# Performance work log

Measured on AMD Instinct MI355X. Metric: run time of the kernel, lower is better.

The kernel has to match this reference:

```python
import jax, jax.numpy as jnp
import numpy as np

B, N, C = 4, 2048, 1024
H = 16
D = C // H  # head dim = 64

def setup_inputs() -> dict:
    key = jax.random.key(0)
    k1, k2, k3 = jax.random.split(key, 3)
    x = jax.random.normal(k1, (B, N, C), dtype=jnp.float32)
    w_attn = jax.random.normal(k2, (C, 3 * C), dtype=jnp.float32) * (C ** -0.5)
    w_proj = jax.random.normal(k3, (C, C), dtype=jnp.float32) * (C ** -0.5)
    return {"x": x, "w_attn": w_attn, "w_proj": w_proj}

def reference(x, w_attn, w_proj):
    # fused QKV projection (bias=False)
    qkv = jnp.einsum('bnc,cf->bnf', x, w_attn)            # [B,N,3C]
    q, k, v = jnp.split(qkv, 3, axis=-1)                  # each [B,N,C]
    # [B,H,N,D]
    q = q.reshape(B, N, H, D).transpose(0, 2, 1, 3)
    k = k.reshape(B, N, H, D).transpose(0, 2, 1, 3)
    v = v.reshape(B, N, H, D).transpose(0, 2, 1, 3)
    # scaled dot-product attention, non-causal, no mask, dropout_p=0
    scale = 1.0 / jnp.sqrt(jnp.asarray(D, dtype=q.dtype))
    scores = jnp.einsum('bhqd,bhkd->bhqk', q, k) * scale  # [B,H,N,N]
    attn = jax.nn.softmax(scores, axis=-1)
    y = jnp.einsum('bhqk,bhkd->bhqd', attn, v)            # [B,H,N,D]
    y = y.transpose(0, 2, 1, 3).reshape(B, N, C)
    # output projection (bias=False); resid dropout is identity at p=0
    return jnp.einsum('bnc,co->bno', y, w_proj)
```

## Files before the change

kernel.cpp:

```cpp
#include <hip/hip_runtime.h>
#include <hip/hip_bf16.h>

typedef __hip_bfloat16 bf16;
typedef short short8 __attribute__((ext_vector_type(8)));
typedef float f32x4 __attribute__((ext_vector_type(4)));
typedef float f32x16 __attribute__((ext_vector_type(16)));

#define GLOBAL_AS __attribute__((address_space(1)))
#define LDS_AS __attribute__((address_space(3)))

__device__ inline unsigned short f2bf(float x) {
    union { float f; unsigned u; } v; v.f = x;
    unsigned r = v.u + 0x7fffu + ((v.u >> 16) & 1u);
    return (unsigned short)(r >> 16);
}

__device__ inline unsigned pkbf(float a, float b) {
    float2 f; f.x = a; f.y = b;
    union { __hip_bfloat162 h; unsigned u; } c;
    c.h = __float22bfloat162_rn(f);
    return c.u;
}

__device__ inline float fast_exp2(float x) {
#if __has_builtin(__builtin_amdgcn_exp2f)
    return __builtin_amdgcn_exp2f(x);
#else
    return exp2f(x);
#endif
}

__device__ inline void async16(const void* g, void* l) {
    __builtin_amdgcn_global_load_lds((const GLOBAL_AS void*)g, (LDS_AS void*)l, 16, 0, 0);
}


__global__ __launch_bounds__(256) void cvt_f32_bf16(const float* __restrict__ in,
                                                    unsigned short* __restrict__ out, int n4) {
    int i = blockIdx.x * 256 + threadIdx.x;
    if (i < n4) {
        float4 v = ((const float4*)in)[i];
        ushort4 o;
        o.x = f2bf(v.x); o.y = f2bf(v.y); o.z = f2bf(v.z); o.w = f2bf(v.w);
        ((ushort4*)out)[i] = o;
    }
}

__global__ __launch_bounds__(256) void transpose_bf16(const float* __restrict__ in,
                                                      unsigned short* __restrict__ out,
                                                      int R, int Cc) {
    __shared__ float s[32][33];
    int tx = threadIdx.x & 31, ty = threadIdx.x >> 5;
    int c0 = blockIdx.x * 32, r0 = blockIdx.y * 32;
#pragma unroll
    for (int i = 0; i < 4; i++)
        s[ty + i * 8][tx] = in[(size_t)(r0 + ty + i * 8) * Cc + c0 + tx];
    __syncthreads();
#pragma unroll
    for (int i = 0; i < 4; i++)
        out[(size_t)(c0 + ty + i * 8) * R + r0 + tx] = f2bf(s[tx][ty + i * 8]);
}


template <int MODE>
__global__ __launch_bounds__(256) void gemm_bf16(const bf16* __restrict__ A,
                                                 const bf16* __restrict__ Bt,
                                                 unsigned short* __restrict__ outQ,
                                                 unsigned short* __restrict__ outK,
                                                 unsigned short* __restrict__ outV,
                                                 float* __restrict__ outF, float qscale) {
    const int KD = 1024;
    __shared__ __align__(16) char smem[34816];
    bf16* sA = (bf16*)smem;
    bf16* sB = (bf16*)(smem + 16384);
    const int t = threadIdx.x;
    const int w = t >> 6, lane = t & 63, l15 = lane & 15, qd = lane >> 4;
    const int bn = blockIdx.x, bm = blockIdx.y;
    const int wm = (w >> 1) * 64, wn = (w & 1) * 64;
    const int sw = l15 & 7;

    f32x4 acc[4][4];
#pragma unroll
    for (int i = 0; i < 4; i++)
#pragma unroll
        for (int j = 0; j < 4; j++) acc[i][j] = (f32x4){0.f, 0.f, 0.f, 0.f};

    const int rsub = lane >> 3;
    const int csrc = ((lane & 7) ^ rsub) << 3;
    const bf16* Ab = A + (size_t)(bm * 128 + w * 32 + rsub) * KD + csrc;
    const bf16* Bb = Bt + (size_t)(bn * 128 + w * 32 + rsub) * KD + csrc;
    bf16* sAw = sA + (w * 32) * 64;
    bf16* sBw = sB + (w * 32) * 64;

    for (int kt = 0; kt < 16; ++kt) {
#pragma unroll
        for (int j = 0; j < 4; ++j) {
            async16(Ab + (size_t)(j * 8) * KD + kt * 64, sAw + j * 512);
            async16(Bb + (size_t)(j * 8) * KD + kt * 64, sBw + j * 512);
        }
        __syncthreads();
#pragma unroll
        for (int ks = 0; ks < 2; ++ks) {
            const int cphys = (((ks * 4 + qd) ^ sw) << 3);
            short8 af[4], bfv[4];
#pragma unroll
            for (int mi = 0; mi < 4; mi++)
                af[mi] = *(const short8*)&sA[(wm + mi * 16 + l15) * 64 + cphys];
#pragma unroll
            for (int ni = 0; ni < 4; ni++)
                bfv[ni] = *(const short8*)&sB[(wn + ni * 16 + l15) * 64 + cphys];
#pragma unroll
            for (int mi = 0; mi < 4; mi++)
#pragma unroll
                for (int ni = 0; ni < 4; ni++)
                    acc[mi][ni] = __builtin_amdgcn_mfma_f32_16x16x32_bf16(af[mi], bfv[ni],
                                                                          acc[mi][ni], 0, 0, 0);
        }
        __syncthreads();
    }

    if (MODE == 0) {
        unsigned short* sC = (unsigned short*)smem;
        const int part = bn >> 3;
        const int hb = (bn & 7) * 2;
        if (part < 2) {
            const float sc = (part == 0) ? qscale : 1.0f;
            unsigned short* dst = (part == 0) ? outQ : outK;
#pragma unroll
            for (int mi = 0; mi < 4; mi++)
#pragma unroll
                for (int ni = 0; ni < 4; ni++)
#pragma unroll
                    for (int r = 0; r < 4; r++)
                        sC[(wm + mi * 16 + qd * 4 + r) * 136 + wn + ni * 16 + l15] =
                            f2bf(acc[mi][ni][r] * sc);
            __syncthreads();
#pragma unroll
            for (int i = 0; i < 8; i++) {
                const int j = t + i * 256;
                const int row = j >> 4, c16 = j & 15;
                uint4 v = *(const uint4*)&sC[row * 136 + c16 * 8];
                const int m = bm * 128 + row;
                const int b = m >> 11, ns = m & 2047;
                const int h = hb + (c16 >> 3);
                const int dd = (c16 & 7) * 8;
                *(uint4*)&dst[((size_t)(b * 16 + h) * 2048 + ns) * 64 + dd] = v;
            }
        } else {
#pragma unroll
            for (int ni = 0; ni < 4; ni++)
#pragma unroll
                for (int mi = 0; mi < 4; mi++) {
                    uint2 pk;
                    pk.x = (unsigned)f2bf(acc[mi][ni][0]) | ((unsigned)f2bf(acc[mi][ni][1]) << 16);
                    pk.y = (unsigned)f2bf(acc[mi][ni][2]) | ((unsigned)f2bf(acc[mi][ni][3]) << 16);
                    *(uint2*)&sC[(wn + ni * 16 + l15) * 136 + wm + mi * 16 + qd * 4] = pk;
                }
            __syncthreads();
            const int m0b = bm * 128;
            const int b = m0b >> 11, ns0 = m0b & 2047;
#pragma unroll
            for (int i = 0; i < 8; i++) {
                const int j = t + i * 256;
                const int f = j >> 4, tc = j & 15;
                uint4 v = *(const uint4*)&sC[f * 136 + tc * 8];
                const int h = hb + (f >> 6), dd = f & 63;
                *(uint4*)&outV[((size_t)(b * 16 + h) * 64 + dd) * 2048 + ns0 + tc * 8] = v;
            }
        }
    } else {
        float* sF = (float*)smem;
#pragma unroll
        for (int pass = 0; pass < 2; ++pass) {
            if (pass) __syncthreads();
            if ((wm >> 6) == pass) {
#pragma unroll
                for (int mi = 0; mi < 4; mi++)
#pragma unroll
                    for (int ni = 0; ni < 4; ni++)
#pragma unroll
                        for (int r = 0; r < 4; r++)
                            sF[(mi * 16 + qd * 4 + r) * 132 + wn + ni * 16 + l15] =
                                acc[mi][ni][r];
            }
            __syncthreads();
#pragma unroll
            for (int i = 0; i < 8; i++) {
                const int j = t + i * 256;
                const int row = j >> 5, c4 = j & 31;
                float4 v = *(const float4*)&sF[row * 132 + c4 * 4];
                *(float4*)&outF[(size_t)(bm * 128 + pass * 64 + row) * 1024 + bn * 128 +
                                c4 * 4] = v;
            }
        }
    }
}


__global__ __launch_bounds__(256) void attn_kernel(const bf16* __restrict__ Q,
                                                   const bf16* __restrict__ K,
                                                   const bf16* __restrict__ Vt,
                                                   bf16* __restrict__ Y) {
    const int blk = blockIdx.x;
    const int bh = (blk & 7) * 8 + (blk >> 7);
    const int qt = (blk >> 3) & 15;
    const int b = bh >> 4, h16 = bh & 15;
    const int t = threadIdx.x, w = t >> 6, lane = t & 63;
    const int c = lane & 31, hl = lane >> 5;
    const int sw = c & 7;

    __shared__ __align__(16) char smem[32768];
    bf16* sK = (bf16*)smem;
    bf16* sVt = (bf16*)(smem + 16384);
    bf16* sO = (bf16*)smem;

    const size_t bhbase = (size_t)bh * 2048 * 64;

    short8 qf[4];
#pragma unroll
    for (int kc = 0; kc < 4; kc++)
        qf[kc] = *(const short8*)(Q + bhbase + (size_t)(qt * 128 + w * 32 + c) * 64 +
                                  kc * 16 + hl * 8);

    f32x16 ot[2];
#pragma unroll
    for (int i = 0; i < 16; i++) { ot[0][i] = 0.f; ot[1][i] = 0.f; }
    float l_run = 0.f;

    const int rsub = lane >> 3;
    const bf16* Kb = K + bhbase + (size_t)(w * 32 + rsub) * 64 + (((lane & 7) ^ rsub) << 3);
    bf16* sKw = sK + (w * 32) * 64;
    const int dsub = lane >> 4, cch = lane & 15;
    const bf16* Vb = Vt + bhbase;

    for (int kt = 0; kt < 16; ++kt) {
#pragma unroll
        for (int j = 0; j < 4; ++j)
            async16(Kb + (size_t)kt * 8192 + j * 512, sKw + j * 512);
#pragma unroll
        for (int j = 0; j < 4; ++j) {
            const int d = w * 16 + j * 4 + dsub;
            async16(Vb + (size_t)d * 2048 + kt * 128 + ((cch ^ (d & 7)) << 3),
                    sVt + (w * 16 + j * 4) * 128);
        }
        __syncthreads();

#pragma unroll
        for (int kt2 = 0; kt2 < 4; ++kt2) {
            f32x16 accS;
#pragma unroll
            for (int i = 0; i < 16; i++) accS[i] = 0.f;
#pragma unroll
            for (int kc = 0; kc < 4; kc++) {
                short8 kf =
                    *(const short8*)&sK[(kt2 * 32 + c) * 64 + (((kc * 2 + hl) ^ sw) << 3)];
                accS = __builtin_amdgcn_mfma_f32_32x32x16_bf16(kf, qf[kc], accS, 0, 0, 0);
            }
            unsigned u[8];
            float ls = 0.f;
#pragma unroll
            for (int i = 0; i < 8; i++) {
                float p0 = fast_exp2(accS[2 * i]);
                float p1 = fast_exp2(accS[2 * i + 1]);
                ls += p0 + p1;
                u[i] = pkbf(p0, p1);
            }
            l_run += ls;
            union { uint4 u4; short8 s8; } F[2];
            F[0].u4.x = u[0]; F[0].u4.y = u[1]; F[0].u4.z = u[2]; F[0].u4.w = u[3];
            F[1].u4.x = u[4]; F[1].u4.y = u[5]; F[1].u4.z = u[6]; F[1].u4.w = u[7];
#pragma unroll
            for (int g = 0; g < 2; ++g) {
#pragma unroll
                for (int mi2 = 0; mi2 < 2; mi2++) {
                    const bf16* vr = &sVt[(mi2 * 32 + c) * 128];
                    uint2 a0 = *(const uint2*)&vr[(((kt2 * 4 + 2 * g) ^ sw) << 3) + hl * 4];
                    uint2 a1 =
                        *(const uint2*)&vr[(((kt2 * 4 + 2 * g + 1) ^ sw) << 3) + hl * 4];
                    union { uint4 u4; short8 s8; } vf;
                    vf.u4.x = a0.x; vf.u4.y = a0.y; vf.u4.z = a1.x; vf.u4.w = a1.y;
                    ot[mi2] =
                        __builtin_amdgcn_mfma_f32_32x32x16_bf16(vf.s8, F[g].s8, ot[mi2], 0, 0, 0);
                }
            }
        }
        __syncthreads();
    }

    float l = l_run + __shfl_xor(l_run, 32, 64);
    float rl = 1.f / l;
#pragma unroll
    for (int mi2 = 0; mi2 < 2; mi2++)
#pragma unroll
        for (int q4 = 0; q4 < 4; q4++) {
            const int d0 = mi2 * 32 + q4 * 8 + hl * 4;
            uint2 pk;
            pk.x = pkbf(ot[mi2][q4 * 4 + 0] * rl, ot[mi2][q4 * 4 + 1] * rl);
            pk.y = pkbf(ot[mi2][q4 * 4 + 2] * rl, ot[mi2][q4 * 4 + 3] * rl);
            *(uint2*)&sO[(w * 32 + c) * 72 + d0] = pk;
        }
    __syncthreads();
#pragma unroll
    for (int i = 0; i < 4; i++) {
        int row = (t >> 3) + i * 32, doff = (t & 7) * 8;
        uint4 vv = *(const uint4*)&sO[row * 72 + doff];
        *(uint4*)(Y + ((size_t)(b * 2048 + qt * 128 + row)) * 1024 + h16 * 64 + doff) = vv;
    }
}


extern "C" void kernel_launch(void* const* d_in, const int* in_sizes, int n_in,
                              void* d_out, int out_size, void* d_ws, size_t ws_size,
                              hipStream_t stream) {
    const float* x = (const float*)d_in[0];
    const float* w_attn = (const float*)d_in[1];
    const float* w_proj = (const float*)d_in[2];
    float* out = (float*)d_out;
    char* ws = (char*)d_ws;

    bf16* xb = (bf16*)(ws);
    bf16* waT = (bf16*)(ws + 16777216);
    bf16* wpT = (bf16*)(ws + 23068672);
    bf16* qb = (bf16*)(ws + 25165824);
    bf16* kb = (bf16*)(ws + 41943040);
    bf16* vtb = (bf16*)(ws + 58720256);

    cvt_f32_bf16<<<8192, 256, 0, stream>>>(x, (unsigned short*)xb, 2097152);
    transpose_bf16<<<dim3(96, 32), 256, 0, stream>>>(w_attn, (unsigned short*)waT, 1024, 3072);
    transpose_bf16<<<dim3(32, 32), 256, 0, stream>>>(w_proj, (unsigned short*)wpT, 1024, 1024);

    const float qscale = 0.125f * 1.44269504088896340736f;
    gemm_bf16<0><<<dim3(24, 64), 256, 0, stream>>>(xb, waT, (unsigned short*)qb,
                                                   (unsigned short*)kb, (unsigned short*)vtb,
                                                   nullptr, qscale);
    attn_kernel<<<dim3(1024), 256, 0, stream>>>(qb, kb, vtb, xb );
    gemm_bf16<1><<<dim3(8, 64), 256, 0, stream>>>(xb, wpT, nullptr, nullptr, nullptr, out, 1.0f);
}
```

Before: 280.0 us.

## Double-buffer K/V tiles in attention kernel to overlap loads with MFMA

Doubles the LDS allocation to hold two K and two V^T tile buffers. The next tile's async copy is issued right after the barrier, so it overlaps with compute on the current tile, and each iteration now needs one barrier instead of two. The row-sum accumulation is also split into two partial sums to shorten the dependency chain. Using 64KB of LDS per block may cut the number of blocks that fit on a CU.

```diff
diff --git a/kernel.cpp b/kernel.cpp
--- a/kernel.cpp
+++ b/kernel.cpp
@@ -209,9 +209,7 @@
     const int c = lane & 31, hl = lane >> 5;
     const int sw = c & 7;
 
-    __shared__ __align__(16) char smem[32768];
-    bf16* sK = (bf16*)smem;
-    bf16* sVt = (bf16*)(smem + 16384);
+    __shared__ __align__(16) char smem[65536];
     bf16* sO = (bf16*)smem;
 
     const size_t bhbase = (size_t)bh * 2048 * 64;
@@ -229,21 +227,40 @@
 
     const int rsub = lane >> 3;
     const bf16* Kb = K + bhbase + (size_t)(w * 32 + rsub) * 64 + (((lane & 7) ^ rsub) << 3);
-    bf16* sKw = sK + (w * 32) * 64;
     const int dsub = lane >> 4, cch = lane & 15;
     const bf16* Vb = Vt + bhbase;
-
-    for (int kt = 0; kt < 16; ++kt) {
-#pragma unroll
-        for (int j = 0; j < 4; ++j)
-            async16(Kb + (size_t)kt * 8192 + j * 512, sKw + j * 512);
+    const int kwoff = (w * 32) * 64;
+
+    {
+        bf16* dK = (bf16*)(smem) + kwoff;
+        bf16* dV = (bf16*)(smem + 32768);
+#pragma unroll
+        for (int j = 0; j < 4; ++j) async16(Kb + j * 512, dK + j * 512);
 #pragma unroll
         for (int j = 0; j < 4; ++j) {
             const int d = w * 16 + j * 4 + dsub;
-            async16(Vb + (size_t)d * 2048 + kt * 128 + ((cch ^ (d & 7)) << 3),
-                    sVt + (w * 16 + j * 4) * 128);
-        }
+            async16(Vb + (size_t)d * 2048 + ((cch ^ (d & 7)) << 3),
+                    dV + (w * 16 + j * 4) * 128);
+        }
+    }
+
+    for (int kt = 0; kt < 16; ++kt) {
         __syncthreads();
+        if (kt < 15) {
+            bf16* dK = (bf16*)(smem + ((kt + 1) & 1) * 16384) + kwoff;
+            bf16* dV = (bf16*)(smem + 32768 + ((kt + 1) & 1) * 16384);
+#pragma unroll
+            for (int j = 0; j < 4; ++j)
+                async16(Kb + (size_t)(kt + 1) * 8192 + j * 512, dK + j * 512);
+#pragma unroll
+            for (int j = 0; j < 4; ++j) {
+                const int d = w * 16 + j * 4 + dsub;
+                async16(Vb + (size_t)d * 2048 + (kt + 1) * 128 + ((cch ^ (d & 7)) << 3),
+                        dV + (w * 16 + j * 4) * 128);
+            }
+        }
+        const bf16* sK = (const bf16*)(smem + (kt & 1) * 16384);
+        const bf16* sVt = (const bf16*)(smem + 32768 + (kt & 1) * 16384);
 
 #pragma unroll
         for (int kt2 = 0; kt2 < 4; ++kt2) {
@@ -257,15 +274,16 @@
                 accS = __builtin_amdgcn_mfma_f32_32x32x16_bf16(kf, qf[kc], accS, 0, 0, 0);
             }
             unsigned u[8];
-            float ls = 0.f;
+            float2 ls2; ls2.x = 0.f; ls2.y = 0.f;
 #pragma unroll
             for (int i = 0; i < 8; i++) {
                 float p0 = fast_exp2(accS[2 * i]);
                 float p1 = fast_exp2(accS[2 * i + 1]);
-                ls += p0 + p1;
+                ls2.x += p0;
+                ls2.y += p1;
                 u[i] = pkbf(p0, p1);
             }
-            l_run += ls;
+            l_run += ls2.x + ls2.y;
             union { uint4 u4; short8 s8; } F[2];
             F[0].u4.x = u[0]; F[0].u4.y = u[1]; F[0].u4.z = u[2]; F[0].u4.w = u[3];
             F[1].u4.x = u[4]; F[1].u4.y = u[5]; F[1].u4.z = u[6]; F[1].u4.w = u[7];
@@ -284,8 +302,8 @@
                 }
             }
         }
-        __syncthreads();
-    }
+    }
+    __syncthreads();
 
     float l = l_run + __shfl_xor(l_run, 32, 64);
     float rl = 1.f / l;
```

Result: slower. 288.6 us (+3.1%).
